# Kernel tuning notes

Measured on AMD Instinct MI355X. Metric: run time of the kernel, lower is better.

Reference implementation:

```python
import jax, jax.numpy as jnp
import numpy as np

B, C, N, H = 8, 256, 1024, 8

def setup_inputs() -> dict:
    key = jax.random.key(0)
    ks = jax.random.split(key, 6)
    x = jax.random.normal(ks[0], (B, C, 3, N), jnp.float32)
    scale = 1.0 / np.sqrt(C).astype(np.float32)
    Wq = jax.random.normal(ks[1], (C, C), jnp.float32) * scale
    Wk = jax.random.normal(ks[2], (C, C), jnp.float32) * scale
    Wv = jax.random.normal(ks[3], (C, C), jnp.float32) * scale
    Wp = jax.random.normal(ks[4], (C, C), jnp.float32) * scale
    mask = jax.random.randint(ks[5], (B, N), 0, 2).astype(bool)  # True = padded
    return {"x": x, "Wq": Wq, "Wk": Wk, "Wv": Wv, "Wp": Wp, "mask": mask}

def _vn_linear(W, x):
    # VNLinear: channel-mixing linear (no bias) over the C axis of [B, C, 3, N]
    return jnp.einsum('oc,bcdn->bodn', W, x)

def _to_heads(t):
    # [B, C, 3, N] -> [B, H, N, (C//H)*3]
    hd = C // H
    return t.reshape(B, H, hd, 3, N).transpose(0, 1, 4, 2, 3).reshape(B, H, N, hd * 3)

def reference(x, Wq, Wk, Wv, Wp, mask):
    hd = C // H
    D = hd * 3
    q = _to_heads(_vn_linear(Wq, x))
    k = _to_heads(_vn_linear(Wk, x))
    v = _to_heads(_vn_linear(Wv, x))
    att = jnp.einsum('bhnd,bhmd->bhnm', q, k) * (1.0 / np.sqrt(D).astype(np.float32))
    att = jnp.where(mask[:, None, None, :], -jnp.inf, att)
    att = jax.nn.softmax(att, axis=-1)
    y = jnp.einsum('bhnm,bhmd->bhnd', att, v)
    # [B, H, N, D] -> [B, H, D, N] -> [B, H, hd, 3, N] -> [B, C, 3, N]
    y = y.transpose(0, 1, 3, 2).reshape(B, H, hd, 3, N).reshape(B, C, 3, N)
    return _vn_linear(Wp, y)
```

## Files before the change

### kernel.cpp

```cpp
#include <hip/hip_runtime.h>
#include <hip/hip_bf16.h>
#include <math.h>

#define B_ 8
#define C_ 256
#define N_ 1024
#define H_ 8
#define DH 96
#define BHN (C_*3*N_)
#define SC 0.10206207261596575f
#define SCL2 0.14722193f

typedef _Float16 half8 __attribute__((ext_vector_type(8)));
typedef float f32x4 __attribute__((ext_vector_type(4)));
typedef float f32x16 __attribute__((ext_vector_type(16)));

typedef __attribute__((address_space(1))) void gvoid;
typedef __attribute__((address_space(3))) void lvoid;
__device__ inline void gl_lds16(const _Float16* g, _Float16* l) {
  __builtin_amdgcn_global_load_lds((gvoid*)g, (lvoid*)l, 16, 0, 0);
}

__device__ inline float ex2(float x) { return __builtin_amdgcn_exp2f(x); }

typedef __fp16 fp16x2 __attribute__((ext_vector_type(2)));
union H2U { fp16x2 h2; unsigned u; };
__device__ inline unsigned pkh(float a, float b) {
  H2U x; x.h2 = __builtin_amdgcn_cvt_pkrtz(a, b); return x.u;
}
union PF { half8 v; unsigned u[4]; };

__device__ inline void plswap(unsigned& a, unsigned& b) {
  asm volatile("v_permlane32_swap_b32 %0, %1" : "+v"(a), "+v"(b));
}

__global__ void convw_kernel(const float* __restrict__ Wq,
                             const float* __restrict__ Wk,
                             const float* __restrict__ Wv,
                             const float* __restrict__ Wp,
                             _Float16* __restrict__ Wh,
                             const unsigned* __restrict__ mraw,
                             unsigned long long* __restrict__ mb) {
  int idx = blockIdx.x * 256 + threadIdx.x;
  int e0 = idx * 8;
  const float* src = (e0 < 65536) ? Wq
                   : (e0 < 131072) ? Wk
                   : (e0 < 196608) ? Wv : Wp;
  int off = e0 & 65535;
  float4 a = *(const float4*)&src[off];
  float4 b = *(const float4*)&src[off + 4];
  _Float16 t[8] = {(_Float16)a.x, (_Float16)a.y, (_Float16)a.z, (_Float16)a.w,
                   (_Float16)b.x, (_Float16)b.y, (_Float16)b.z, (_Float16)b.w};
  *(uint4*)&Wh[e0] = *(uint4*)t;

  if (blockIdx.x == 0) {
    __shared__ int notI, notF;
    if (threadIdx.x == 0) { notI = 0; notF = 0; }
    __syncthreads();
    int li = 0, lf = 0;
    for (int i = threadIdx.x; i < 2048; i += 256) {
      unsigned w = mraw[i];
      if (w > 1u) li = 1;
      if (w != 0u && w != 0x3F800000u) lf = 1;
    }
    if (li) atomicOr(&notI, 1);
    if (lf) atomicOr(&notF, 1);
    __syncthreads();
    const int tid = threadIdx.x;
    if (tid < 128) {
      int base = tid * 64;
      unsigned long long bits = 0;
      if (!notI) {
        for (int j = 0; j < 64; ++j)
          bits |= (unsigned long long)(mraw[base + j] & 1u) << j;
      } else if (!notF) {
        for (int j = 0; j < 64; ++j)
          bits |= (unsigned long long)(mraw[base + j] != 0u ? 1 : 0) << j;
      } else {
        const unsigned char* m8 = (const unsigned char*)mraw;
        for (int j = 0; j < 64; ++j)
          bits |= (unsigned long long)(m8[base + j] ? 1 : 0) << j;
      }
      mb[tid] = bits;
    }
  }
}

__global__ __launch_bounds__(256) void convxt_kernel(
    const float* __restrict__ x, _Float16* __restrict__ XT) {
  __shared__ _Float16 T[64][65];
  const int m0 = blockIdx.x * 64;
  const int c0 = blockIdx.y * 64;
  const int b = blockIdx.z;
  const float* xb = x + (size_t)b * BHN;
  _Float16* ob = XT + (size_t)b * BHN;
  const int t = threadIdx.x;
#pragma unroll
  for (int i = 0; i < 16; ++i) {
    int e = t + i * 256;
    int c = e >> 6, m = e & 63;
    T[m][c] = (_Float16)xb[(size_t)(c0 + c) * 3072 + m0 + m];
  }
  __syncthreads();
#pragma unroll
  for (int i = 0; i < 2; ++i) {
    int e = t + i * 256;
    int m = e >> 3, ch = e & 7;
    _Float16 tmp[8];
#pragma unroll
    for (int j = 0; j < 8; ++j) tmp[j] = T[m][ch * 8 + j];
    *(uint4*)&ob[(size_t)(m0 + m) * 256 + c0 + ch * 8] = *(uint4*)tmp;
  }
}

template <int MODE>
__global__ __launch_bounds__(256, 4) void mgemm_kernel(
    const _Float16* __restrict__ Wh, int woff,
    const _Float16* __restrict__ Xn,
    _Float16* __restrict__ O0, _Float16* __restrict__ O1,
    _Float16* __restrict__ O2, float* __restrict__ Of, int nw) {
  const int zz = blockIdx.z;
  const int w = zz % nw;
  const int b = zz / nw;
  const _Float16* Wb = Wh + (size_t)(woff + w) * 65536;
  const _Float16* Bb = Xn + (size_t)b * BHN;
  const int o0 = blockIdx.y * 128;
  const int bn0 = blockIdx.x * 128;

  __shared__ __align__(16) _Float16 Ah[4096];
  __shared__ __align__(16) _Float16 Bh[4096];

  const int tid = threadIdx.x;
  const int wave = tid >> 6;
  const int lane = tid & 63;
  const int lg = lane >> 4, ll = lane & 15;
  const int wm = wave >> 1, wn = wave & 1;
  const int r0 = tid >> 2, c4 = tid & 3;

  f32x4 acc[4][4];
#pragma unroll
  for (int mi = 0; mi < 4; ++mi)
#pragma unroll
    for (int ni = 0; ni < 4; ++ni) acc[mi][ni] = (f32x4){0.f, 0.f, 0.f, 0.f};

  for (int k0 = 0; k0 < 256; k0 += 32) {
    gl_lds16(Wb + (size_t)(o0 + r0) * 256 + k0 + c4 * 8, &Ah[wave * 512]);
    gl_lds16(Wb + (size_t)(o0 + 64 + r0) * 256 + k0 + c4 * 8,
             &Ah[2048 + wave * 512]);
    gl_lds16(Bb + (size_t)(bn0 + r0) * 256 + k0 + c4 * 8, &Bh[wave * 512]);
    gl_lds16(Bb + (size_t)(bn0 + 64 + r0) * 256 + k0 + c4 * 8,
             &Bh[2048 + wave * 512]);
    __syncthreads();
    half8 af[4], bf[4];
#pragma unroll
    for (int mi = 0; mi < 4; ++mi)
      af[mi] = *(const half8*)&Ah[(wm * 64 + mi * 16 + ll) * 32 + lg * 8];
#pragma unroll
    for (int ni = 0; ni < 4; ++ni)
      bf[ni] = *(const half8*)&Bh[(wn * 64 + ni * 16 + ll) * 32 + lg * 8];
#pragma unroll
    for (int mi = 0; mi < 4; ++mi)
#pragma unroll
      for (int ni = 0; ni < 4; ++ni)
        acc[mi][ni] = __builtin_amdgcn_mfma_f32_16x16x32_f16(
            af[mi], bf[ni], acc[mi][ni], 0, 0, 0);
    __syncthreads();
  }

#pragma unroll
  for (int mi = 0; mi < 4; ++mi) {
#pragma unroll
    for (int ni = 0; ni < 4; ++ni) {
      int o = o0 + wm * 64 + mi * 16 + lg * 4;
      int mcol = bn0 + wn * 64 + ni * 16 + ll;
      if constexpr (MODE == 1) {
        float* Ofb = Of + (size_t)b * BHN;
#pragma unroll
        for (int r = 0; r < 4; ++r)
          Ofb[(size_t)(o + r) * 3072 + mcol] = acc[mi][ni][r];
      } else {
        const int h = o >> 5, i = o & 31;
        const int dd = mcol >> 10, tok = mcol & 1023;
        const size_t bh8 = (size_t)(b * 8 + h);
        if (w == 2) {
          int tt = tok >> 6, kk = tok & 63;
          int kt = kk >> 4, hi2 = (kk >> 3) & 1, e = kk & 7;
          size_t base = ((((bh8 * 16 + tt) * 4 + kt) * 3 + dd) * 512) +
                        (size_t)i * 16 + hi2 * 8 + e;
#pragma unroll
          for (int r = 0; r < 4; ++r)
            O2[base + r * 16] = (_Float16)acc[mi][ni][r];
        } else {
          int dperm = dd * 32 + i;
          int pp = dperm >> 3, j0 = i & 7;
          int ks = pp >> 1, hif = pp & 1;
          float qs = (w == 0) ? SCL2 : 1.0f;
          _Float16 t4[4];
#pragma unroll
          for (int r = 0; r < 4; ++r) t4[r] = (_Float16)(acc[mi][ni][r] * qs);
          size_t idx;
          if (w == 0) {
            idx = ((bh8 * 32 + (tok >> 5)) * 6 + ks) * 512 +
                  (size_t)(tok & 31) * 16 + hif * 8 + j0;
            *(uint2*)&O0[idx] = *(uint2*)t4;
          } else {
            idx = ((bh8 * 16 + (tok >> 6)) * 6 + ks) * 1024 +
                  (size_t)(tok & 63) * 16 + hif * 8 + j0;
            *(uint2*)&O1[idx] = *(uint2*)t4;
          }
        }
      }
    }
  }
}

__global__ __launch_bounds__(256, 2) void attn_kernel(
    const _Float16* __restrict__ Qp, const _Float16* __restrict__ Kp,
    const _Float16* __restrict__ Vp,
    const unsigned long long* __restrict__ mbits,
    _Float16* __restrict__ yT) {
  const int gid = blockIdx.x;
  const int bh = gid & 63;
  const int qt = gid >> 6;
  const int b = bh >> 3, h = bh & 7;
  const int n0 = qt * 128;

  const int tid = threadIdx.x;
  const int lane = tid & 63;
  const int wave = tid >> 6;
  const int hi = lane >> 5;
  const int lq = lane & 31;
  const int wq0 = wave * 32;

  const size_t bh8 = (size_t)(b * 8 + h);
  const int lo16 = lq * 16 + hi * 8;

  const _Float16* Qb = Qp + (bh8 * 32 + (qt * 4 + wave)) * 6 * 512 + lo16;
  half8 qf[6];
#pragma unroll
  for (int ks = 0; ks < 6; ++ks) qf[ks] = *(const half8*)(Qb + ks * 512);

  const _Float16* Kh = Kp + bh8 * 98304 + lo16;
  const _Float16* Vh = Vp + bh8 * 98304 + lo16;

  half8 kf[6][2];
  auto loadK = [&](int t) {
    const _Float16* Kt = Kh + t * 6144;
#pragma unroll
    for (int ks = 0; ks < 6; ++ks) {
      kf[ks][0] = *(const half8*)(Kt + ks * 1024);
      kf[ks][1] = *(const half8*)(Kt + ks * 1024 + 512);
    }
  };
  loadK(0);

  float M = 0.f, Lh = 0.f;
  f32x16 yacc[3];
#pragma unroll
  for (int dt = 0; dt < 3; ++dt)
#pragma unroll
    for (int r = 0; r < 16; ++r) yacc[dt][r] = 0.f;

#pragma unroll 2
  for (int t = 0; t < 16; ++t) {
    const _Float16* Vt = Vh + t * 6144;
    half8 vf[4][3];
#pragma unroll
    for (int kt = 0; kt < 4; ++kt)
#pragma unroll
      for (int dt = 0; dt < 3; ++dt)
        vf[kt][dt] = *(const half8*)(Vt + (kt * 3 + dt) * 512);

    const unsigned long long m64 = mbits[b * 16 + t];

    f32x16 s[2];
#pragma unroll
    for (int r = 0; r < 16; ++r) { s[0][r] = 0.f; s[1][r] = 0.f; }
    __builtin_amdgcn_s_setprio(1);
#pragma unroll
    for (int ks = 0; ks < 6; ++ks) {
      s[0] = __builtin_amdgcn_mfma_f32_32x32x16_f16(kf[ks][0], qf[ks], s[0],
                                                    0, 0, 0);
      s[1] = __builtin_amdgcn_mfma_f32_32x32x16_f16(kf[ks][1], qf[ks], s[1],
                                                    0, 0, 0);
    }
    __builtin_amdgcn_s_setprio(0);

    if (t + 1 < 16) loadK(t + 1);

    float mx = -1e30f;
#pragma unroll
    for (int nt = 0; nt < 2; ++nt) {
      unsigned wm = (unsigned)(m64 >> (nt * 32 + 4 * hi));
#pragma unroll
      for (int r = 0; r < 16; ++r) {
        float sv = s[nt][r];
        sv = ((wm >> ((r & 3) + 8 * (r >> 2))) & 1u) ? -1e30f : sv;
        s[nt][r] = sv;
        mx = fmaxf(mx, sv);
      }
    }
    if (__any(mx > M + 12.f)) {
      float mx2 = fmaxf(mx, __shfl_xor(mx, 32));
      float newM = fmaxf(M, mx2);
      float corr = ex2(M - newM);
      M = newM;
      Lh *= corr;
#pragma unroll
      for (int dt = 0; dt < 3; ++dt)
#pragma unroll
        for (int r = 0; r < 16; ++r) yacc[dt][r] *= corr;
    }
    float psum = 0.f;
#pragma unroll
    for (int nt = 0; nt < 2; ++nt)
#pragma unroll
      for (int r = 0; r < 16; ++r) {
        float p = ex2(s[nt][r] - M);
        s[nt][r] = p;
        psum += p;
      }
    Lh += psum;

    unsigned pw[4][4];
#pragma unroll
    for (int nt = 0; nt < 2; ++nt)
#pragma unroll
      for (int hf = 0; hf < 2; ++hf) {
        const int bs = hf * 8;
        unsigned A0 = pkh(s[nt][bs + 0], s[nt][bs + 1]);
        unsigned A1 = pkh(s[nt][bs + 2], s[nt][bs + 3]);
        unsigned B0 = pkh(s[nt][bs + 4], s[nt][bs + 5]);
        unsigned B1 = pkh(s[nt][bs + 6], s[nt][bs + 7]);
        plswap(A0, B0);
        plswap(A1, B1);
        pw[nt * 2 + hf][0] = A0;
        pw[nt * 2 + hf][1] = A1;
        pw[nt * 2 + hf][2] = B0;
        pw[nt * 2 + hf][3] = B1;
      }

    __builtin_amdgcn_s_setprio(1);
#pragma unroll
    for (int kt = 0; kt < 4; ++kt) {
      PF pf;
      pf.u[0] = pw[kt][0];
      pf.u[1] = pw[kt][1];
      pf.u[2] = pw[kt][2];
      pf.u[3] = pw[kt][3];
#pragma unroll
      for (int dt = 0; dt < 3; ++dt)
        yacc[dt] = __builtin_amdgcn_mfma_f32_32x32x16_f16(
            vf[kt][dt], pf.v, yacc[dt], 0, 0, 0);
    }
    __builtin_amdgcn_s_setprio(0);
  }

  float L = Lh + __shfl_xor(Lh, 32);
  float inv = (L > 0.f) ? 1.f / L : 0.f;
  _Float16* yb = yT + (size_t)b * BHN;
#pragma unroll
  for (int dt = 0; dt < 3; ++dt) {
    _Float16* rowp =
        yb + (size_t)(dt * 1024 + n0 + wq0 + lq) * 256 + h * 32 + hi * 4;
#pragma unroll
    for (int g = 0; g < 4; ++g) {
      _Float16 t4[4];
#pragma unroll
      for (int j = 0; j < 4; ++j)
        t4[j] = (_Float16)(yacc[dt][g * 4 + j] * inv);
      *(uint2*)(rowp + g * 8) = *(uint2*)t4;
    }
  }
}

extern "C" void kernel_launch(void* const* d_in, const int* in_sizes, int n_in,
                              void* d_out, int out_size, void* d_ws,
                              size_t ws_size, hipStream_t stream) {
  const float* x = (const float*)d_in[0];
  const float* Wq = (const float*)d_in[1];
  const float* Wk = (const float*)d_in[2];
  const float* Wv = (const float*)d_in[3];
  const float* Wp = (const float*)d_in[4];
  const unsigned* mask = (const unsigned*)d_in[5];
  float* out = (float*)d_out;

  _Float16* Wh = (_Float16*)d_ws;
  _Float16* XT = Wh + 4 * 65536;
  _Float16* Qp = XT + (size_t)B_ * BHN;
  _Float16* Kp = Qp + (size_t)B_ * BHN;
  _Float16* Vp = Kp + (size_t)B_ * BHN;
  _Float16* yT = Vp + (size_t)B_ * BHN;
  unsigned long long* mb = (unsigned long long*)(yT + (size_t)B_ * BHN);

  convw_kernel<<<128, 256, 0, stream>>>(Wq, Wk, Wv, Wp, Wh, mask, mb);
  convxt_kernel<<<dim3(48, 4, B_), 256, 0, stream>>>(x, XT);

  dim3 g1(24, 2, B_ * 3);
  mgemm_kernel<0><<<g1, 256, 0, stream>>>(Wh, 0, XT, Qp, Kp, Vp, nullptr, 3);

  attn_kernel<<<dim3(512), 256, 0, stream>>>(Qp, Kp, Vp, mb, yT);

  dim3 g3(24, 2, B_);
  mgemm_kernel<1><<<g3, 256, 0, stream>>>(Wh, 3, yT, nullptr, nullptr, nullptr,
                                          out, 1);
}
```

Baseline: 91.11 us.

## Use additive mask as MFMA accumulator init and compute row sums via MFMA

The padding mask becomes a precomputed additive float tensor laid out in the MFMA accumulator order. The attention kernel loads it directly as the initial QK^T accumulator, which removes the per-element bit-test selects. The softmax denominator is now accumulated by an extra MFMA against a ones vector instead of scalar adds and a cross-lane shuffle, and the max reduction is written as a tree. This removes VALU work from the softmax path but adds one MFMA per key sub-tile, 16 more accumulator registers and more global mask traffic per tile.

Measured after the change: 113.1 us. 1.24x slower.

```diff
diff --git a/kernel.cpp b/kernel.cpp
--- a/kernel.cpp
+++ b/kernel.cpp
@@ -40,7 +40,7 @@
                              const float* __restrict__ Wp,
                              _Float16* __restrict__ Wh,
                              const unsigned* __restrict__ mraw,
-                             unsigned long long* __restrict__ mb) {
+                             float* __restrict__ Madd) {
   int idx = blockIdx.x * 256 + threadIdx.x;
   int e0 = idx * 8;
   const float* src = (e0 < 65536) ? Wq
@@ -69,19 +69,17 @@
     const int tid = threadIdx.x;
     if (tid < 128) {
       int base = tid * 64;
-      unsigned long long bits = 0;
-      if (!notI) {
-        for (int j = 0; j < 64; ++j)
-          bits |= (unsigned long long)(mraw[base + j] & 1u) << j;
-      } else if (!notF) {
-        for (int j = 0; j < 64; ++j)
-          bits |= (unsigned long long)(mraw[base + j] != 0u ? 1 : 0) << j;
-      } else {
-        const unsigned char* m8 = (const unsigned char*)mraw;
-        for (int j = 0; j < 64; ++j)
-          bits |= (unsigned long long)(m8[base + j] ? 1 : 0) << j;
+      const unsigned char* m8 = (const unsigned char*)mraw;
+      for (int j = 0; j < 64; ++j) {
+        int pad;
+        if (!notI)      pad = (int)(mraw[base + j] & 1u);
+        else if (!notF) pad = (mraw[base + j] != 0u) ? 1 : 0;
+        else            pad = m8[base + j] ? 1 : 0;
+        int nt = j >> 5, rem = j & 31;
+        int hi = (rem >> 2) & 1;
+        int r = (rem & 3) + 4 * (rem >> 3);
+        Madd[((tid * 2 + nt) * 2 + hi) * 16 + r] = pad ? -1e30f : 0.f;
       }
-      mb[tid] = bits;
     }
   }
 }
@@ -216,8 +214,7 @@
 
 __global__ __launch_bounds__(256, 2) void attn_kernel(
     const _Float16* __restrict__ Qp, const _Float16* __restrict__ Kp,
-    const _Float16* __restrict__ Vp,
-    const unsigned long long* __restrict__ mbits,
+    const _Float16* __restrict__ Vp, const float* __restrict__ Madd,
     _Float16* __restrict__ yT) {
   const int gid = blockIdx.x;
   const int bh = gid & 63;
@@ -242,6 +239,7 @@
 
   const _Float16* Kh = Kp + bh8 * 98304 + lo16;
   const _Float16* Vh = Vp + bh8 * 98304 + lo16;
+  const float* Mb = Madd + (b * 16) * 64 + hi * 16;
 
   half8 kf[6][2];
   auto loadK = [&](int t) {
@@ -254,12 +252,18 @@
   };
   loadK(0);
 
-  float M = 0.f, Lh = 0.f;
-  f32x16 yacc[3];
+  half8 ones;
+#pragma unroll
+  for (int j = 0; j < 8; ++j) ones[j] = (_Float16)1.0f;
+
+  float M = 0.f;
+  f32x16 yacc[3], Lacc;
 #pragma unroll
   for (int dt = 0; dt < 3; ++dt)
 #pragma unroll
     for (int r = 0; r < 16; ++r) yacc[dt][r] = 0.f;
+#pragma unroll
+  for (int r = 0; r < 16; ++r) Lacc[r] = 0.f;
 
 #pragma unroll 2
   for (int t = 0; t < 16; ++t) {
@@ -271,11 +275,10 @@
       for (int dt = 0; dt < 3; ++dt)
         vf[kt][dt] = *(const half8*)(Vt + (kt * 3 + dt) * 512);
 
-    const unsigned long long m64 = mbits[b * 16 + t];
-
     f32x16 s[2];
-#pragma unroll
-    for (int r = 0; r < 16; ++r) { s[0][r] = 0.f; s[1][r] = 0.f; }
+    s[0] = *(const f32x16*)(Mb + t * 64);
+    s[1] = *(const f32x16*)(Mb + t * 64 + 32);
+
     __builtin_amdgcn_s_setprio(1);
 #pragma unroll
     for (int ks = 0; ks < 6; ++ks) {
@@ -288,39 +291,31 @@
 
     if (t + 1 < 16) loadK(t + 1);
 
-    float mx = -1e30f;
-#pragma unroll
-    for (int nt = 0; nt < 2; ++nt) {
-      unsigned wm = (unsigned)(m64 >> (nt * 32 + 4 * hi));
-#pragma unroll
-      for (int r = 0; r < 16; ++r) {
-        float sv = s[nt][r];
-        sv = ((wm >> ((r & 3) + 8 * (r >> 2))) & 1u) ? -1e30f : sv;
-        s[nt][r] = sv;
-        mx = fmaxf(mx, sv);
-      }
-    }
+    float m8a[8];
+#pragma unroll
+    for (int r = 0; r < 8; ++r)
+      m8a[r] = fmaxf(fmaxf(s[0][r], s[0][r + 8]),
+                     fmaxf(s[1][r], s[1][r + 8]));
+    float m4a = fmaxf(m8a[0], m8a[4]), m4b = fmaxf(m8a[1], m8a[5]);
+    float m4c = fmaxf(m8a[2], m8a[6]), m4d = fmaxf(m8a[3], m8a[7]);
+    float mx = fmaxf(fmaxf(m4a, m4b), fmaxf(m4c, m4d));
+
     if (__any(mx > M + 12.f)) {
       float mx2 = fmaxf(mx, __shfl_xor(mx, 32));
       float newM = fmaxf(M, mx2);
       float corr = ex2(M - newM);
       M = newM;
-      Lh *= corr;
+#pragma unroll
+      for (int r = 0; r < 16; ++r) Lacc[r] *= corr;
 #pragma unroll
       for (int dt = 0; dt < 3; ++dt)
 #pragma unroll
         for (int r = 0; r < 16; ++r) yacc[dt][r] *= corr;
     }
-    float psum = 0.f;
 #pragma unroll
     for (int nt = 0; nt < 2; ++nt)
 #pragma unroll
-      for (int r = 0; r < 16; ++r) {
-        float p = ex2(s[nt][r] - M);
-        s[nt][r] = p;
-        psum += p;
-      }
-    Lh += psum;
+      for (int r = 0; r < 16; ++r) s[nt][r] = ex2(s[nt][r] - M);
 
     unsigned pw[4][4];
 #pragma unroll
@@ -348,6 +343,7 @@
       pf.u[1] = pw[kt][1];
       pf.u[2] = pw[kt][2];
       pf.u[3] = pw[kt][3];
+      Lacc = __builtin_amdgcn_mfma_f32_32x32x16_f16(ones, pf.v, Lacc, 0, 0, 0);
 #pragma unroll
       for (int dt = 0; dt < 3; ++dt)
         yacc[dt] = __builtin_amdgcn_mfma_f32_32x32x16_f16(
@@ -356,7 +352,7 @@
     __builtin_amdgcn_s_setprio(0);
   }
 
-  float L = Lh + __shfl_xor(Lh, 32);
+  float L = Lacc[0];
   float inv = (L > 0.f) ? 1.f / L : 0.f;
   _Float16* yb = yT + (size_t)b * BHN;
 #pragma unroll
@@ -391,15 +387,15 @@
   _Float16* Kp = Qp + (size_t)B_ * BHN;
   _Float16* Vp = Kp + (size_t)B_ * BHN;
   _Float16* yT = Vp + (size_t)B_ * BHN;
-  unsigned long long* mb = (unsigned long long*)(yT + (size_t)B_ * BHN);
-
-  convw_kernel<<<128, 256, 0, stream>>>(Wq, Wk, Wv, Wp, Wh, mask, mb);
+  float* Madd = (float*)(yT + (size_t)B_ * BHN);
+
+  convw_kernel<<<128, 256, 0, stream>>>(Wq, Wk, Wv, Wp, Wh, mask, Madd);
   convxt_kernel<<<dim3(48, 4, B_), 256, 0, stream>>>(x, XT);
 
   dim3 g1(24, 2, B_ * 3);
   mgemm_kernel<0><<<g1, 256, 0, stream>>>(Wh, 0, XT, Qp, Kp, Vp, nullptr, 3);
 
-  attn_kernel<<<dim3(512), 256, 0, stream>>>(Qp, Kp, Vp, mb, yT);
+  attn_kernel<<<dim3(512), 256, 0, stream>>>(Qp, Kp, Vp, Madd, yT);
 
   dim3 g3(24, 2, B_);
   mgemm_kernel<1><<<g3, 256, 0, stream>>>(Wh, 3, yT, nullptr, nullptr, nullptr,
```

## Split key range across two wave groups in attention and merge via LDS

Applied to the files above, without the earlier changes.

The attention block grows to 512 threads, with two groups of four waves each processing half of the key tiles for the same query rows. Partial outputs, running max and sum from the second group are written to shared memory and merged by the first group using log-sum-exp rescaling. This raises wave-level parallelism per block to hide latency, at the cost of a combine step and a tighter launch bound that may force register spills.

Measured after the change: 297.4 us. +226.4%, slower.

```diff
diff --git a/kernel.cpp b/kernel.cpp
--- a/kernel.cpp
+++ b/kernel.cpp
@@ -214,7 +214,7 @@
   }
 }
 
-__global__ __launch_bounds__(256, 2) void attn_kernel(
+__global__ __launch_bounds__(512, 4) void attn_kernel(
     const _Float16* __restrict__ Qp, const _Float16* __restrict__ Kp,
     const _Float16* __restrict__ Vp,
     const unsigned long long* __restrict__ mbits,
@@ -225,17 +225,22 @@
   const int b = bh >> 3, h = bh & 7;
   const int n0 = qt * 128;
 
+  __shared__ float CB[4 * 64 * 56];
+
   const int tid = threadIdx.x;
   const int lane = tid & 63;
   const int wave = tid >> 6;
+  const int qsub = wave & 3;
+  const int half = wave >> 2;
   const int hi = lane >> 5;
   const int lq = lane & 31;
-  const int wq0 = wave * 32;
+  const int wq0 = qsub * 32;
+  const int t0 = half * 8;
 
   const size_t bh8 = (size_t)(b * 8 + h);
   const int lo16 = lq * 16 + hi * 8;
 
-  const _Float16* Qb = Qp + (bh8 * 32 + (qt * 4 + wave)) * 6 * 512 + lo16;
+  const _Float16* Qb = Qp + (bh8 * 32 + (qt * 4 + qsub)) * 6 * 512 + lo16;
   half8 qf[6];
 #pragma unroll
   for (int ks = 0; ks < 6; ++ks) qf[ks] = *(const half8*)(Qb + ks * 512);
@@ -252,7 +257,7 @@
       kf[ks][1] = *(const half8*)(Kt + ks * 1024 + 512);
     }
   };
-  loadK(0);
+  loadK(t0);
 
   float M = 0.f, Lh = 0.f;
   f32x16 yacc[3];
@@ -261,8 +266,7 @@
 #pragma unroll
     for (int r = 0; r < 16; ++r) yacc[dt][r] = 0.f;
 
-#pragma unroll 2
-  for (int t = 0; t < 16; ++t) {
+  for (int t = t0; t < t0 + 8; ++t) {
     const _Float16* Vt = Vh + t * 6144;
     half8 vf[4][3];
 #pragma unroll
@@ -286,7 +290,7 @@
     }
     __builtin_amdgcn_s_setprio(0);
 
-    if (t + 1 < 16) loadK(t + 1);
+    if (t + 1 < t0 + 8) loadK(t + 1);
 
     float mx = -1e30f;
 #pragma unroll
@@ -356,20 +360,43 @@
     __builtin_amdgcn_s_setprio(0);
   }
 
-  float L = Lh + __shfl_xor(Lh, 32);
-  float inv = (L > 0.f) ? 1.f / L : 0.f;
-  _Float16* yb = yT + (size_t)b * BHN;
-#pragma unroll
-  for (int dt = 0; dt < 3; ++dt) {
-    _Float16* rowp =
-        yb + (size_t)(dt * 1024 + n0 + wq0 + lq) * 256 + h * 32 + hi * 4;
-#pragma unroll
-    for (int g = 0; g < 4; ++g) {
-      _Float16 t4[4];
-#pragma unroll
-      for (int j = 0; j < 4; ++j)
-        t4[j] = (_Float16)(yacc[dt][g * 4 + j] * inv);
-      *(uint2*)(rowp + g * 8) = *(uint2*)t4;
+  float Lown = Lh + __shfl_xor(Lh, 32);
+  if (wave >= 4) {
+    int base = ((wave - 4) * 64 + lane) * 56;
+#pragma unroll
+    for (int dt = 0; dt < 3; ++dt)
+#pragma unroll
+      for (int g = 0; g < 4; ++g)
+        *(f32x4*)&CB[base + dt * 16 + g * 4] =
+            (f32x4){yacc[dt][g * 4 + 0], yacc[dt][g * 4 + 1],
+                    yacc[dt][g * 4 + 2], yacc[dt][g * 4 + 3]};
+    CB[base + 48] = M;
+    CB[base + 49] = Lown;
+  }
+  __syncthreads();
+  if (wave < 4) {
+    int base = (wave * 64 + lane) * 56;
+    float Mb = CB[base + 48], Lb = CB[base + 49];
+    float newM = fmaxf(M, Mb);
+    float ca = ex2(M - newM), cb = ex2(Mb - newM);
+    float L = Lown * ca + Lb * cb;
+    float inv = (L > 0.f) ? 1.f / L : 0.f;
+    _Float16* yb = yT + (size_t)b * BHN;
+#pragma unroll
+    for (int dt = 0; dt < 3; ++dt) {
+      _Float16* rowp =
+          yb + (size_t)(dt * 1024 + n0 + wq0 + lq) * 256 + h * 32 + hi * 4;
+#pragma unroll
+      for (int g = 0; g < 4; ++g) {
+        _Float16 t4[4];
+#pragma unroll
+        for (int j = 0; j < 4; ++j) {
+          float yo = yacc[dt][g * 4 + j] * ca +
+                     CB[base + dt * 16 + g * 4 + j] * cb;
+          t4[j] = (_Float16)(yo * inv);
+        }
+        *(uint2*)(rowp + g * 8) = *(uint2*)t4;
+      }
     }
   }
 }
@@ -399,7 +426,7 @@
   dim3 g1(24, 2, B_ * 3);
   mgemm_kernel<0><<<g1, 256, 0, stream>>>(Wh, 0, XT, Qp, Kp, Vp, nullptr, 3);
 
-  attn_kernel<<<dim3(512), 256, 0, stream>>>(Qp, Kp, Vp, mb, yT);
+  attn_kernel<<<dim3(512), 512, 0, stream>>>(Qp, Kp, Vp, mb, yT);
 
   dim3 g3(24, 2, B_);
   mgemm_kernel<1><<<g3, 256, 0, stream>>>(Wh, 3, yT, nullptr, nullptr, nullptr,
```
